# Optimization experiments

Measured on AMD Instinct MI355X. Metric: run time of the kernel, lower is better.

## Reference

```python
import jax, jax.numpy as jnp
from jax import lax
import numpy as np

MAX_VIEWS = 200
IGNORE_LABEL = -1
PERM_SEED = 0


def _plan(predict_np, max_views=MAX_VIEWS, ignore_label=IGNORE_LABEL, seed=PERM_SEED):
    """Host-side replication of _hard_anchor_sampling's integer index logic.

    Returns per-(image,class) padded pixel-index tables, validity masks, the
    random n_view-subset indices (torch.randperm equivalent), n_view, and
    classes_index (unique non-ignore classes across the batch, pre-filter).
    """
    B, N = predict_np.shape
    per = []  # (image_id, class_id, pixel_indices)
    classes_index = set()
    for ii in range(B):
        vals, counts = np.unique(predict_np[ii], return_counts=True)
        for v in vals:
            if v != ignore_label:
                classes_index.add(int(v))
        for v, c in zip(vals, counts):
            if v == ignore_label or c < max_views:
                continue
            per.append((ii, int(v), np.nonzero(predict_np[ii] == v)[0]))
    assert per, 'no class reaches max_views'
    n_view = int(min(len(idx) for _, _, idx in per))
    P = len(per)
    M = int(max(len(idx) for _, _, idx in per))
    rng = np.random.default_rng(seed)
    img_ids = np.array([p[0] for p in per], dtype=np.int32)
    cls_ids = np.array([p[1] for p in per], dtype=np.int32)
    idx_pad = np.zeros((P, M), dtype=np.int32)
    valid = np.zeros((P, M), dtype=bool)
    sel = np.zeros((P, n_view), dtype=np.int32)
    for p, (ii, v, idx) in enumerate(per):
        L = len(idx)
        idx_pad[p, :L] = idx
        idx_pad[p, L:] = idx[0]
        valid[p, :L] = True
        perm = rng.permutation(L)[:n_view]  # torch.randperm(num_easy)[:n_view]
        sel[p] = idx[perm]
    classes_index = np.array(sorted(classes_index), dtype=np.int32)
    return img_ids, cls_ids, idx_pad, valid, sel, n_view, classes_index


def setup_inputs() -> dict:
    key = jax.random.key(0)
    k1, k2, k3 = jax.random.split(key, 3)
    feats = jax.random.normal(k1, (8, 256, 128, 128), dtype=jnp.float32)
    labels = jax.random.randint(k2, (8, 128, 128), 0, 16, dtype=jnp.int64)
    predict = jax.random.randint(k3, (8, 16384), 0, 16, dtype=jnp.int64)
    return {'feats': feats, 'labels': labels, 'predict': predict}


def _forward(feats, predict_plan):
    img_ids, cls_ids, idx_pad, valid, sel, n_view, classes_index = predict_plan
    B, C, H, W = feats.shape
    feats_flat = jnp.transpose(feats, (0, 2, 3, 1)).reshape(B, H * W, C)

    # ---- hard anchor sampling (vectorized over all (image,class) slots) ----
    # padded gather of all pixels of each class: [P, M, C]
    X_easy = feats_flat[img_ids[:, None], idx_pad]
    top2 = lax.top_k(X_easy, 2)[0]                      # [P, M, 2] over channels
    certainty = top2[..., 0] - top2[..., 1]             # [P, M]
    certainty = jnp.where(valid, certainty, -jnp.inf)   # mask padding
    k = int(n_view // 2)
    _, best = lax.top_k(certainty, k)                   # [P, k]
    X_cert = jnp.take_along_axis(X_easy, best[..., None], axis=1)  # [P, k, C]
    X_cert = X_cert.mean(axis=1)                        # averaged certainty feature
    X_sel = feats_flat[img_ids[:, None], sel]           # [P, n_view, C]
    X_ = jnp.concatenate([X_sel, X_cert[:, None, :]], axis=1)  # [P, n_view+1, C]

    # ---- contrastive loss ----
    f = X_[:, :, classes_index]                         # [P, n_view+1, D]
    D = f.shape[-1]
    pos_all = f[:, :-1, :].reshape(-1, D)
    pos = jnp.broadcast_to(f[:, -1:, :], f[:, :-1, :].shape).reshape(-1, D)
    # CosineEmbeddingLoss with target=1 -> 1 - cos_sim (margin irrelevant)
    eps = 1e-8
    cos_sim = jnp.sum(pos_all * pos, -1) / jnp.maximum(
        jnp.linalg.norm(pos_all, axis=-1) * jnp.linalg.norm(pos, axis=-1), eps)
    class_inter_loss = jnp.mean(1.0 - cos_sim)

    pos_ = f[:, -1, :]                                  # [P, D]
    sim = pos_ @ pos_.T
    nrm = jnp.sqrt(jnp.sum(pos_ ** 2, axis=1))
    cosm = sim / (nrm[:, None] * nrm[None, :])
    cls = jnp.asarray(cls_ids)
    mask = (cls[:, None] != cls[None, :]).astype(f.dtype)  # equal->0, unequal->1
    class_intra_loss = jnp.sum((cosm + 1.0) * mask) / jnp.sum(mask)
    return class_intra_loss + class_inter_loss


def reference(feats, labels, predict):
    # labels is interpolated (nearest) to feats' HxW then passed as y_hat, which
    # _hard_anchor_sampling never reads; here labels already matches HxW.
    plan = _plan(np.asarray(predict))
    return _forward(feats, plan)
```

## Files before the change

kernel.cpp:

```cpp
#include <hip/hip_runtime.h>
#include <math.h>

#define BB 8
#define NCLS 16
#define NPIX 16384
#define CHN 256
#define MAXV 200
#define SORTN 2048

typedef unsigned long long ull;


__device__ __forceinline__ void build_plan(const int* __restrict__ counts2,
                                           int* __restrict__ plan, int tid) {
    __shared__ int c[128];
    __shared__ int sc[128];
    __shared__ int mn[128];
    __shared__ int present[NCLS];
    int* chan = plan + 4;
    int* pimg = plan + 20;
    int* pcls = plan + 148;
    int* pmap = plan + 276;
    int* Lp   = plan + 404;
    if (tid < 128) {
        int b = tid >> 4, v = tid & 15;
        int s = 0;
        for (int j = 0; j < 64; ++j) s += counts2[((b << 6) + j) * NCLS + v];
        c[tid] = s;
    }
    if (tid < NCLS) present[tid] = 0;
    __syncthreads();
    int e = 0;
    if (tid < 128) {
        if (c[tid] > 0) atomicOr(&present[tid & 15], 1);
        e = (c[tid] >= MAXV) ? 1 : 0;
        sc[tid] = e;
        mn[tid] = e ? c[tid] : 0x7fffffff;
    }
    __syncthreads();
    for (int off = 1; off < 128; off <<= 1) {
        int add = 0;
        if (tid < 128 && tid >= off) add = sc[tid - off];
        __syncthreads();
        if (tid < 128) sc[tid] += add;
        __syncthreads();
    }
    for (int s = 64; s > 0; s >>= 1) {
        if (tid < s) mn[tid] = min(mn[tid], mn[tid + s]);
        __syncthreads();
    }
    if (tid < 128) {
        pmap[tid] = e ? (sc[tid] - 1) : -1;
        if (e) {
            int p = sc[tid] - 1;
            pimg[p] = tid >> 4; pcls[p] = tid & 15; Lp[p] = c[tid];
        }
    }
    if (tid == 0) {
        int D = 0;
        for (int v = 0; v < NCLS; ++v) if (present[v]) chan[D++] = v;
        int nview = mn[0];
        plan[0] = nview; plan[1] = nview / 2; plan[2] = sc[127]; plan[3] = D;
    }
}

template <int NC>
__global__ __launch_bounds__(256) void k_cert1h(const float* __restrict__ feats,
                                                const int* __restrict__ predict,
                                                float2* __restrict__ part,
                                                int* __restrict__ counts2) {
    int bid = blockIdx.x;
    int tid = threadIdx.x;
    if (bid < 512) {
        __shared__ int h[NCLS];
        if (tid < NCLS) h[tid] = 0;
        __syncthreads();
        int v = predict[bid * 256 + tid];
        if (v >= 0 && v < NCLS) atomicAdd(&h[v], 1);
        __syncthreads();
        if (tid < NCLS) counts2[bid * NCLS + tid] = h[tid];
    }
    int chunk = bid % NC;
    int tile  = (bid / NC) % 16;
    int b     = bid / (NC * 16);
    int n4 = tile * 1024 + tid * 4;
    const float* fb = feats + (size_t)b * CHN * NPIX + n4;
    int c0 = chunk * (CHN / NC);
    float m1[4] = {-INFINITY, -INFINITY, -INFINITY, -INFINITY};
    float m2[4] = {-INFINITY, -INFINITY, -INFINITY, -INFINITY};
    for (int cb = c0; cb < c0 + CHN / NC; cb += 8) {
        float4 xs[8];
#pragma unroll
        for (int u = 0; u < 8; ++u)
            xs[u] = *(const float4*)(fb + (size_t)(cb + u) * NPIX);
#pragma unroll
        for (int u = 0; u < 8; ++u) {
            float xv[4] = {xs[u].x, xs[u].y, xs[u].z, xs[u].w};
#pragma unroll
            for (int q = 0; q < 4; ++q) {
                float val = xv[q];
                if (val > m1[q]) { m2[q] = m1[q]; m1[q] = val; }
                else if (val > m2[q]) m2[q] = val;
            }
        }
    }
    float2* po = part + (((size_t)(b * NC + chunk)) << 14) + n4;
#pragma unroll
    for (int q = 0; q < 4; ++q) po[q] = make_float2(m1[q], m2[q]);
}

template <int NC>
__global__ __launch_bounds__(256) void k_cert2p(const float2* __restrict__ part,
                                                const int* __restrict__ counts2,
                                                float* __restrict__ cert,
                                                int* __restrict__ plan) {
    int tid = threadIdx.x;
    if (blockIdx.x == 512) {
        build_plan(counts2, plan, tid);
        return;
    }
    int t = blockIdx.x * 256 + tid;
    int b = t >> 14, pix = t & (NPIX - 1);
    float2 pm[NC];
#pragma unroll
    for (int j = 0; j < NC; ++j)
        pm[j] = part[(((size_t)(b * NC + j)) << 14) + pix];
    float m1 = -INFINITY, m2 = -INFINITY;
#pragma unroll
    for (int j = 0; j < NC; ++j) {
        if (pm[j].x > m1) { m2 = fmaxf(m1, pm[j].y); m1 = pm[j].x; }
        else              { m2 = fmaxf(m2, pm[j].x); }
    }
    cert[t] = m1 - m2;
}

__global__ __launch_bounds__(512) void k_sel(const int* __restrict__ predict,
                                             const float* __restrict__ cert,
                                             const int* __restrict__ plan,
                                             ull* __restrict__ thrKey,
                                             float* __restrict__ pos_sum) {
    __shared__ ull keys[SORTN];
    __shared__ int whist[8][256];
    __shared__ int scan[257];
    __shared__ int wtot[4];
    __shared__ int lcnt;
    __shared__ ull sprefix;
    __shared__ int sremain;
    __shared__ int sdone;
    int tid = threadIdx.x;
    if (blockIdx.x == 0) {
#pragma unroll
        for (int i = 0; i < 4; ++i) pos_sum[i * 512 + tid] = 0.f;
    }
    int lane = tid & 63, wv = tid >> 6;
    int b = blockIdx.x >> 4, v = blockIdx.x & 15;
    const int* pmap = plan + 276;
    int p = pmap[b * NCLS + v];
    if (p < 0) return;
    if (tid == 0) { lcnt = 0; sprefix = 0; sdone = 0; }
    __syncthreads();
    for (int n = tid; n < NPIX; n += 512) {
        bool match = (predict[b * NPIX + n] == v);
        ull mask = __ballot(match);
        if (mask) {
            int leader = __ffsll((long long)mask) - 1;
            int basepos = 0;
            if (lane == leader) basepos = atomicAdd(&lcnt, __popcll(mask));
            basepos = __shfl(basepos, leader, 64);
            if (match) {
                int pos = basepos + __popcll(mask & ((1ull << lane) - 1));
                if (pos < SORTN) {
                    unsigned int m = __float_as_uint(cert[b * NPIX + n]) | 0x80000000u;
                    keys[pos] = ((ull)m << 32) | (ull)(0xFFFFFFFFu - (unsigned)n);
                }
            }
        }
    }
    __syncthreads();
    int L = lcnt < SORTN ? lcnt : SORTN;
    int kv = plan[1] < L ? plan[1] : L;
    if (tid == 0) sremain = kv;
    __syncthreads();
    for (int shift = 56; shift >= 0; shift -= 8) {
        if (sdone) break;
        for (int i = tid; i < 8 * 256; i += 512) ((int*)whist)[i] = 0;
        ull pref = sprefix;
        int rem = sremain;
        __syncthreads();
        ull maskHi = (shift == 56) ? 0ULL : (~0ULL) << (shift + 8);
        for (int i = tid; i < L; i += 512) {
            ull kk = keys[i];
            if ((kk & maskHi) == pref)
                atomicAdd(&whist[wv][(int)((kk >> shift) & 255)], 1);
        }
        __syncthreads();
        int s = 0;
        if (tid < 256) {
            for (int w = 0; w < 8; ++w) s += whist[w][tid];
            for (int off = 1; off < 64; off <<= 1) {
                int o = __shfl_down(s, off, 64);
                if (lane + off < 64) s += o;
            }
            if (lane == 0) wtot[wv] = s;
        }
        __syncthreads();
        if (tid < 256) {
            int offs = 0;
            for (int w2 = wv + 1; w2 < 4; ++w2) offs += wtot[w2];
            s += offs;
            scan[tid] = s;
            if (tid == 0) scan[256] = 0;
        }
        __syncthreads();
        if (tid < 256) {
            int nxt = scan[tid + 1];
            if (s >= rem && nxt < rem) {
                sprefix = pref | ((ull)tid << shift);
                sremain = rem - nxt;
                if (s == rem) sdone = 1;
            }
        }
        __syncthreads();
    }
    if (tid == 0) thrKey[p] = sprefix;
}

__global__ __launch_bounds__(512) void k_accum(const float* __restrict__ feats,
                                               const int* __restrict__ predict,
                                               const float* __restrict__ cert,
                                               const int* __restrict__ plan,
                                               const ull* __restrict__ thrKey,
                                               float* __restrict__ pos_sum) {
    __shared__ float gacc[NCLS * 16];
    int tid = threadIdx.x;
    int t = blockIdx.x * 512 + tid;
    int b = (blockIdx.x * 512) >> 14;
    int n = t & (NPIX - 1);
    const int* chan = plan + 4;
    const int* pmap = plan + 276;
    int D = plan[3];
    if (tid < NCLS * 16) gacc[tid] = 0.f;
    __syncthreads();
    int v = predict[t];
    if (v >= 0 && v < NCLS) {
        int p = pmap[b * NCLS + v];
        if (p >= 0) {
            unsigned int m = __float_as_uint(cert[t]) | 0x80000000u;
            ull key = ((ull)m << 32) | (ull)(0xFFFFFFFFu - (unsigned)n);
            if (key >= thrKey[p]) {
                const float* fb = feats + ((size_t)(b * CHN) << 14) + n;
                if (D == 16) {
                    float x[16];
#pragma unroll
                    for (int d = 0; d < 16; ++d)
                        x[d] = fb[(size_t)chan[d] << 14];
#pragma unroll
                    for (int d = 0; d < 16; ++d)
                        atomicAdd(&gacc[v * 16 + d], x[d]);
                } else {
                    for (int d = 0; d < D; ++d)
                        atomicAdd(&gacc[v * 16 + d], fb[(size_t)chan[d] << 14]);
                }
            }
        }
    }
    __syncthreads();
    if (tid < NCLS * 16) {
        int p = pmap[b * NCLS + (tid >> 4)];
        if (p >= 0 && gacc[tid] != 0.f) atomicAdd(&pos_sum[p * 16 + (tid & 15)], gacc[tid]);
    }
}

__global__ __launch_bounds__(256) void k_interintra(const float* __restrict__ feats,
                                                    const int* __restrict__ predict,
                                                    const int* __restrict__ plan,
                                                    const float* __restrict__ pos_sum,
                                                    double* __restrict__ accpart) {
    __shared__ float ppd[128 * 16];
    __shared__ float nr[128];
    __shared__ double red[256];
    int tid = threadIdx.x;
    int P = plan[2], D = plan[3];
    const int* pcls = plan + 148;
    for (int i = tid; i < P * 16; i += 256) ppd[i] = pos_sum[i];
    __syncthreads();
    for (int p = tid; p < P; p += 256) {
        float s = 0;
        for (int d = 0; d < D; ++d) { float x = ppd[p * 16 + d]; s += x * x; }
        nr[p] = sqrtf(s);
    }
    __syncthreads();

    if (blockIdx.x == 512) {
        __shared__ int cl[128];
        for (int p = tid; p < P; p += 256) cl[p] = pcls[p];
        __syncthreads();
        double num = 0; int cnt = 0;
        for (int idx = tid; idx < P * P; idx += 256) {
            int i = idx / P, j = idx - i * P;
            if (cl[i] != cl[j]) {
                float dot = 0;
                for (int d = 0; d < D; ++d) dot += ppd[i * 16 + d] * ppd[j * 16 + d];
                num += (double)(dot / (nr[i] * nr[j])) + 1.0;
                cnt++;
            }
        }
        red[tid] = num; __syncthreads();
        for (int s = 128; s > 0; s >>= 1) { if (tid < s) red[tid] += red[tid + s]; __syncthreads(); }
        double totnum = red[0]; __syncthreads();
        red[tid] = (double)cnt; __syncthreads();
        for (int s = 128; s > 0; s >>= 1) { if (tid < s) red[tid] += red[tid + s]; __syncthreads(); }
        if (tid == 0) accpart[512] = totnum / red[0];
        return;
    }

    int t = blockIdx.x * 256 + tid;
    int b = t >> 14, n = t & (NPIX - 1);
    const int* chan = plan + 4;
    const int* pmap = plan + 276;
    const int* Lp = plan + 404;
    double term = 0;
    int v = predict[t];
    if (v >= 0 && v < NCLS) {
        int p = pmap[b * NCLS + v];
        if (p >= 0) {
            const float* fb = feats + ((size_t)(b * CHN) << 14) + n;
            float dot = 0, nv = 0;
            if (D == 16) {
                float x[16];
#pragma unroll
                for (int d = 0; d < 16; ++d) x[d] = fb[(size_t)chan[d] << 14];
#pragma unroll
                for (int d = 0; d < 16; ++d) {
                    float y = ppd[p * 16 + d];
                    dot += x[d] * y; nv += x[d] * x[d];
                }
            } else {
                for (int d = 0; d < D; ++d) {
                    float x = fb[(size_t)chan[d] << 14];
                    float y = ppd[p * 16 + d];
                    dot += x * y; nv += x * x;
                }
            }
            float den = fmaxf(sqrtf(nv) * nr[p], 1e-8f);
            term = (1.0 - (double)(dot / den)) / ((double)Lp[p] * (double)P);
        }
    }
    red[tid] = term; __syncthreads();
    for (int s = 128; s > 0; s >>= 1) { if (tid < s) red[tid] += red[tid + s]; __syncthreads(); }
    if (tid == 0) accpart[blockIdx.x] = red[0];
}

__global__ __launch_bounds__(256) void k_finish(const double* __restrict__ accpart,
                                                float* __restrict__ out) {
    __shared__ double red[256];
    int tid = threadIdx.x;
    double s = 0;
    for (int i = tid; i < 513; i += 256) s += accpart[i];
    red[tid] = s; __syncthreads();
    for (int st = 128; st > 0; st >>= 1) { if (tid < st) red[tid] += red[tid + st]; __syncthreads(); }
    if (tid == 0) out[0] = (float)red[0];
}

__global__ __launch_bounds__(256) void k_hist(const int* __restrict__ predict,
                                              int* __restrict__ counts2) {
    __shared__ int h[NCLS];
    int tid = threadIdx.x;
    if (tid < NCLS) h[tid] = 0;
    __syncthreads();
    int v = predict[blockIdx.x * 256 + tid];
    if (v >= 0 && v < NCLS) atomicAdd(&h[v], 1);
    __syncthreads();
    if (tid < NCLS) counts2[blockIdx.x * NCLS + tid] = h[tid];
}

__global__ __launch_bounds__(256) void k_plan1(const int* __restrict__ counts2,
                                               int* __restrict__ plan) {
    build_plan(counts2, plan, threadIdx.x);
}

__global__ __launch_bounds__(256) void k_cert_direct(const float* __restrict__ feats,
                                                     float* __restrict__ cert) {
    int t = blockIdx.x * 256 + threadIdx.x;
    int b = t >> 12;
    int n4 = (t & 4095) * 4;
    const float* fb = feats + (size_t)b * CHN * NPIX + n4;
    float m1[4] = {-INFINITY, -INFINITY, -INFINITY, -INFINITY};
    float m2[4] = {-INFINITY, -INFINITY, -INFINITY, -INFINITY};
    for (int cb = 0; cb < CHN; cb += 8) {
        float4 xs[8];
#pragma unroll
        for (int u = 0; u < 8; ++u)
            xs[u] = *(const float4*)(fb + (size_t)(cb + u) * NPIX);
#pragma unroll
        for (int u = 0; u < 8; ++u) {
            float xv[4] = {xs[u].x, xs[u].y, xs[u].z, xs[u].w};
#pragma unroll
            for (int q = 0; q < 4; ++q) {
                float val = xv[q];
                if (val > m1[q]) { m2[q] = m1[q]; m1[q] = val; }
                else if (val > m2[q]) m2[q] = val;
            }
        }
    }
    float4 o = {m1[0] - m2[0], m1[1] - m2[1], m1[2] - m2[2], m1[3] - m2[3]};
    *(float4*)(cert + b * NPIX + n4) = o;
}

extern "C" void kernel_launch(void* const* d_in, const int* in_sizes, int n_in,
                              void* d_out, int out_size, void* d_ws, size_t ws_size,
                              hipStream_t stream) {
    const float* feats  = (const float*)d_in[0];
    const int* predict  = (const int*)d_in[2];
    char* ws = (char*)d_ws;
    double* accpart = (double*)ws;
    int* plan       = (int*)(ws + 8192);
    ull* thrKey     = (ull*)(ws + 12288);
    float* pos_sum  = (float*)(ws + 16384);
    int* counts2    = (int*)(ws + 24576);
    float* cert     = (float*)(ws + 65536);
    float2* part    = (float2*)(ws + 1048576);
    float* out      = (float*)d_out;

    size_t need8 = 1048576 + (size_t)8 * BB * NPIX * sizeof(float2);
    size_t need4 = 1048576 + (size_t)4 * BB * NPIX * sizeof(float2);
    if (ws_size >= need8) {
        k_cert1h<8> <<<BB * 16 * 8, 256, 0, stream>>>(feats, predict, part, counts2);
        k_cert2p<8> <<<513, 256, 0, stream>>>(part, counts2, cert, plan);
    } else if (ws_size >= need4) {
        k_cert1h<4> <<<BB * 16 * 4, 256, 0, stream>>>(feats, predict, part, counts2);
        k_cert2p<4> <<<513, 256, 0, stream>>>(part, counts2, cert, plan);
    } else {
        k_hist <<<512, 256, 0, stream>>>(predict, counts2);
        k_cert_direct <<<128, 256, 0, stream>>>(feats, cert);
        k_plan1 <<<1, 256, 0, stream>>>(counts2, plan);
    }
    k_sel        <<<128, 512, 0, stream>>>(predict, cert, plan, thrKey, pos_sum);
    k_accum      <<<256, 512, 0, stream>>>(feats, predict, cert, plan, thrKey, pos_sum);
    k_interintra <<<513, 256, 0, stream>>>(feats, predict, plan, pos_sum, accpart);
    k_finish     <<<1,   256, 0, stream>>>(accpart, out);
}
```

Baseline: 260.7 us.

## Fuse channel top-2 reduction into one kernel and build plan inside selection

The two-pass certainty computation, which wrote per-chunk partial top-2 values to global memory and reduced them in a second kernel, becomes one kernel. Each block splits the 256 channels across four wavefronts and combines their partial results in shared memory. The plan-building block is folded into k_sel as an extra block, and each selection block recomputes class counts, the minimum count and its plan index from counts2, so it no longer waits for a separate plan kernel. This removes one launch and the global round trip of the partials. In exchange, each block now does a smaller chunk of channel work, and every selection block repeats the count reduction.

```diff
diff --git a/kernel.cpp b/kernel.cpp
--- a/kernel.cpp
+++ b/kernel.cpp
@@ -64,31 +64,28 @@
     }
 }
 
-template <int NC>
-__global__ __launch_bounds__(256) void k_cert1h(const float* __restrict__ feats,
-                                                const int* __restrict__ predict,
-                                                float2* __restrict__ part,
-                                                int* __restrict__ counts2) {
+__global__ __launch_bounds__(256) void k_cert(const float* __restrict__ feats,
+                                              const int* __restrict__ predict,
+                                              float* __restrict__ cert,
+                                              int* __restrict__ counts2) {
+    __shared__ int h[NCLS];
+    __shared__ float2 sh[4 * 256];
     int bid = blockIdx.x;
     int tid = threadIdx.x;
-    if (bid < 512) {
-        __shared__ int h[NCLS];
-        if (tid < NCLS) h[tid] = 0;
-        __syncthreads();
-        int v = predict[bid * 256 + tid];
-        if (v >= 0 && v < NCLS) atomicAdd(&h[v], 1);
-        __syncthreads();
-        if (tid < NCLS) counts2[bid * NCLS + tid] = h[tid];
-    }
-    int chunk = bid % NC;
-    int tile  = (bid / NC) % 16;
-    int b     = bid / (NC * 16);
-    int n4 = tile * 1024 + tid * 4;
-    const float* fb = feats + (size_t)b * CHN * NPIX + n4;
-    int c0 = chunk * (CHN / NC);
+    if (tid < NCLS) h[tid] = 0;
+    __syncthreads();
+    int pv = predict[bid * 256 + tid];
+    if (pv >= 0 && pv < NCLS) atomicAdd(&h[pv], 1);
+
+    int lane = tid & 63;
+    int slice = tid >> 6;
+    int b = bid >> 6;
+    int tile = bid & 63;
+    int n4 = tile * 256 + lane * 4;
+    const float* fb = feats + (size_t)b * CHN * NPIX + (size_t)(slice * 64) * NPIX + n4;
     float m1[4] = {-INFINITY, -INFINITY, -INFINITY, -INFINITY};
     float m2[4] = {-INFINITY, -INFINITY, -INFINITY, -INFINITY};
-    for (int cb = c0; cb < c0 + CHN / NC; cb += 8) {
+    for (int cb = 0; cb < 64; cb += 8) {
         float4 xs[8];
 #pragma unroll
         for (int u = 0; u < 8; ++u)
@@ -104,41 +101,62 @@
             }
         }
     }
-    float2* po = part + (((size_t)(b * NC + chunk)) << 14) + n4;
-#pragma unroll
-    for (int q = 0; q < 4; ++q) po[q] = make_float2(m1[q], m2[q]);
-}
-
-template <int NC>
-__global__ __launch_bounds__(256) void k_cert2p(const float2* __restrict__ part,
-                                                const int* __restrict__ counts2,
-                                                float* __restrict__ cert,
-                                                int* __restrict__ plan) {
-    int tid = threadIdx.x;
-    if (blockIdx.x == 512) {
+#pragma unroll
+    for (int q = 0; q < 4; ++q)
+        sh[slice * 256 + lane * 4 + q] = make_float2(m1[q], m2[q]);
+    __syncthreads();
+    if (tid < NCLS) counts2[bid * NCLS + tid] = h[tid];
+    float M1 = -INFINITY, M2 = -INFINITY;
+#pragma unroll
+    for (int j = 0; j < 4; ++j) {
+        float2 pm = sh[j * 256 + tid];
+        if (pm.x > M1) { M2 = fmaxf(M1, pm.y); M1 = pm.x; }
+        else           { M2 = fmaxf(M2, pm.x); }
+    }
+    cert[bid * 256 + tid] = M1 - M2;
+}
+
+__global__ __launch_bounds__(512) void k_sel(const int* __restrict__ predict,
+                                             const float* __restrict__ cert,
+                                             const int* __restrict__ counts2,
+                                             int* __restrict__ plan,
+                                             ull* __restrict__ thrKey,
+                                             float* __restrict__ pos_sum) {
+    int tid = threadIdx.x;
+    int lane = tid & 63, wv = tid >> 6;
+    if (blockIdx.x == 128) {
+#pragma unroll
+        for (int i = 0; i < 4; ++i) pos_sum[i * 512 + tid] = 0.f;
         build_plan(counts2, plan, tid);
         return;
     }
-    int t = blockIdx.x * 256 + tid;
-    int b = t >> 14, pix = t & (NPIX - 1);
-    float2 pm[NC];
-#pragma unroll
-    for (int j = 0; j < NC; ++j)
-        pm[j] = part[(((size_t)(b * NC + j)) << 14) + pix];
-    float m1 = -INFINITY, m2 = -INFINITY;
-#pragma unroll
-    for (int j = 0; j < NC; ++j) {
-        if (pm[j].x > m1) { m2 = fmaxf(m1, pm[j].y); m1 = pm[j].x; }
-        else              { m2 = fmaxf(m2, pm[j].x); }
-    }
-    cert[t] = m1 - m2;
-}
-
-__global__ __launch_bounds__(512) void k_sel(const int* __restrict__ predict,
-                                             const float* __restrict__ cert,
-                                             const int* __restrict__ plan,
-                                             ull* __restrict__ thrKey,
-                                             float* __restrict__ pos_sum) {
+    __shared__ int cc[128];
+    __shared__ int mnl[128];
+    __shared__ ull em[2];
+    int cv = 0;
+    if (tid < 128) {
+        int b0 = tid >> 4, v0 = tid & 15;
+        int s = 0;
+        for (int j = 0; j < 64; ++j) s += counts2[((b0 << 6) + j) * NCLS + v0];
+        cv = s; cc[tid] = s;
+    }
+    bool e = (tid < 128) && (cv >= MAXV);
+    ull m = __ballot(e);
+    if (lane == 0 && wv < 2) em[wv] = m;
+    if (tid < 128) mnl[tid] = e ? cv : 0x7fffffff;
+    __syncthreads();
+    for (int s = 64; s > 0; s >>= 1) {
+        if (tid < s) mnl[tid] = min(mnl[tid], mnl[tid + s]);
+        __syncthreads();
+    }
+    int bvid = blockIdx.x;
+    if (cc[bvid] < MAXV) return;
+    int kvplan = mnl[0] >> 1;
+    int p = (bvid < 64)
+        ? __popcll(em[0] & ((1ull << bvid) - 1))
+        : __popcll(em[0]) + __popcll(em[1] & ((1ull << (bvid - 64)) - 1));
+    int b = bvid >> 4, v = bvid & 15;
+
     __shared__ ull keys[SORTN];
     __shared__ int whist[8][256];
     __shared__ int scan[257];
@@ -147,16 +165,6 @@
     __shared__ ull sprefix;
     __shared__ int sremain;
     __shared__ int sdone;
-    int tid = threadIdx.x;
-    if (blockIdx.x == 0) {
-#pragma unroll
-        for (int i = 0; i < 4; ++i) pos_sum[i * 512 + tid] = 0.f;
-    }
-    int lane = tid & 63, wv = tid >> 6;
-    int b = blockIdx.x >> 4, v = blockIdx.x & 15;
-    const int* pmap = plan + 276;
-    int p = pmap[b * NCLS + v];
-    if (p < 0) return;
     if (tid == 0) { lcnt = 0; sprefix = 0; sdone = 0; }
     __syncthreads();
     for (int n = tid; n < NPIX; n += 512) {
@@ -170,15 +178,15 @@
             if (match) {
                 int pos = basepos + __popcll(mask & ((1ull << lane) - 1));
                 if (pos < SORTN) {
-                    unsigned int m = __float_as_uint(cert[b * NPIX + n]) | 0x80000000u;
-                    keys[pos] = ((ull)m << 32) | (ull)(0xFFFFFFFFu - (unsigned)n);
+                    unsigned int mm = __float_as_uint(cert[b * NPIX + n]) | 0x80000000u;
+                    keys[pos] = ((ull)mm << 32) | (ull)(0xFFFFFFFFu - (unsigned)n);
                 }
             }
         }
     }
     __syncthreads();
     int L = lcnt < SORTN ? lcnt : SORTN;
-    int kv = plan[1] < L ? plan[1] : L;
+    int kv = kvplan < L ? kvplan : L;
     if (tid == 0) sremain = kv;
     __syncthreads();
     for (int shift = 56; shift >= 0; shift -= 8) {
@@ -362,51 +370,6 @@
     if (tid == 0) out[0] = (float)red[0];
 }
 
-__global__ __launch_bounds__(256) void k_hist(const int* __restrict__ predict,
-                                              int* __restrict__ counts2) {
-    __shared__ int h[NCLS];
-    int tid = threadIdx.x;
-    if (tid < NCLS) h[tid] = 0;
-    __syncthreads();
-    int v = predict[blockIdx.x * 256 + tid];
-    if (v >= 0 && v < NCLS) atomicAdd(&h[v], 1);
-    __syncthreads();
-    if (tid < NCLS) counts2[blockIdx.x * NCLS + tid] = h[tid];
-}
-
-__global__ __launch_bounds__(256) void k_plan1(const int* __restrict__ counts2,
-                                               int* __restrict__ plan) {
-    build_plan(counts2, plan, threadIdx.x);
-}
-
-__global__ __launch_bounds__(256) void k_cert_direct(const float* __restrict__ feats,
-                                                     float* __restrict__ cert) {
-    int t = blockIdx.x * 256 + threadIdx.x;
-    int b = t >> 12;
-    int n4 = (t & 4095) * 4;
-    const float* fb = feats + (size_t)b * CHN * NPIX + n4;
-    float m1[4] = {-INFINITY, -INFINITY, -INFINITY, -INFINITY};
-    float m2[4] = {-INFINITY, -INFINITY, -INFINITY, -INFINITY};
-    for (int cb = 0; cb < CHN; cb += 8) {
-        float4 xs[8];
-#pragma unroll
-        for (int u = 0; u < 8; ++u)
-            xs[u] = *(const float4*)(fb + (size_t)(cb + u) * NPIX);
-#pragma unroll
-        for (int u = 0; u < 8; ++u) {
-            float xv[4] = {xs[u].x, xs[u].y, xs[u].z, xs[u].w};
-#pragma unroll
-            for (int q = 0; q < 4; ++q) {
-                float val = xv[q];
-                if (val > m1[q]) { m2[q] = m1[q]; m1[q] = val; }
-                else if (val > m2[q]) m2[q] = val;
-            }
-        }
-    }
-    float4 o = {m1[0] - m2[0], m1[1] - m2[1], m1[2] - m2[2], m1[3] - m2[3]};
-    *(float4*)(cert + b * NPIX + n4) = o;
-}
-
 extern "C" void kernel_launch(void* const* d_in, const int* in_sizes, int n_in,
                               void* d_out, int out_size, void* d_ws, size_t ws_size,
                               hipStream_t stream) {
@@ -419,23 +382,10 @@
     float* pos_sum  = (float*)(ws + 16384);
     int* counts2    = (int*)(ws + 24576);
     float* cert     = (float*)(ws + 65536);
-    float2* part    = (float2*)(ws + 1048576);
     float* out      = (float*)d_out;
 
-    size_t need8 = 1048576 + (size_t)8 * BB * NPIX * sizeof(float2);
-    size_t need4 = 1048576 + (size_t)4 * BB * NPIX * sizeof(float2);
-    if (ws_size >= need8) {
-        k_cert1h<8> <<<BB * 16 * 8, 256, 0, stream>>>(feats, predict, part, counts2);
-        k_cert2p<8> <<<513, 256, 0, stream>>>(part, counts2, cert, plan);
-    } else if (ws_size >= need4) {
-        k_cert1h<4> <<<BB * 16 * 4, 256, 0, stream>>>(feats, predict, part, counts2);
-        k_cert2p<4> <<<513, 256, 0, stream>>>(part, counts2, cert, plan);
-    } else {
-        k_hist <<<512, 256, 0, stream>>>(predict, counts2);
-        k_cert_direct <<<128, 256, 0, stream>>>(feats, cert);
-        k_plan1 <<<1, 256, 0, stream>>>(counts2, plan);
-    }
-    k_sel        <<<128, 512, 0, stream>>>(predict, cert, plan, thrKey, pos_sum);
+    k_cert       <<<512, 256, 0, stream>>>(feats, predict, cert, counts2);
+    k_sel        <<<129, 512, 0, stream>>>(predict, cert, counts2, plan, thrKey, pos_sum);
     k_accum      <<<256, 512, 0, stream>>>(feats, predict, cert, plan, thrKey, pos_sum);
     k_interintra <<<513, 256, 0, stream>>>(feats, predict, plan, pos_sum, accpart);
     k_finish     <<<1,   256, 0, stream>>>(accpart, out);
```

Result: no change. 256.3 us (-1.7%).
